# Optimization experiments

Measured on AMD Instinct MI355X. Metric: run time of the kernel, lower is better.

The kernel has to match this reference:

```python
import jax, jax.numpy as jnp
import numpy as np

WS = 7          # window size
NUM_HEADS = 8


def _depthwise_conv3x3(x, w, b):
    # x: [B, C, H, W], w: [C, 1, 3, 3], groups=C depthwise, padding=1
    y = jax.lax.conv_general_dilated(
        x, w, window_strides=(1, 1), padding='SAME',
        dimension_numbers=('NCHW', 'OIHW', 'NCHW'),
        feature_group_count=x.shape[1])
    return y + b[None, :, None, None]


def setup_inputs() -> dict:
    key = jax.random.key(0)
    k1, k2, k3 = jax.random.split(key, 3)
    B, H, W, C = 8, 112, 112, 256
    qkv = jax.random.normal(k1, (3, B, H * W, C), dtype=jnp.float32)
    lepe_w = jax.random.normal(k2, (C, 1, 3, 3), dtype=jnp.float32) * 0.1
    lepe_b = jax.random.normal(k3, (C,), dtype=jnp.float32) * 0.1
    return {"qkv": qkv, "lepe_w": lepe_w, "lepe_b": lepe_b, "H": H, "W": W}


def reference(qkv, lepe_w, lepe_b, H, W):
    q, k, v = qkv[0], qkv[1], qkv[2]          # each [B, N, C]
    B, N, C = v.shape
    hd = C // NUM_HEADS
    scale = hd ** -0.5
    Gh, Gw = H // WS, W // WS                 # H, W assumed divisible by WS

    # LePE: depthwise 3x3 conv on v viewed as image
    lepe = _depthwise_conv3x3(v.transpose(0, 2, 1).reshape(B, C, H, W), lepe_w, lepe_b)
    lepe = lepe.reshape(B, C, N).transpose(0, 2, 1)   # [B, N, C]

    def to_windows(x):
        # [B, N, C] -> [B*Gh*Gw, heads, ws*ws, hd]
        x = x.reshape(B, Gh, WS, Gw, WS, NUM_HEADS, hd)
        return x.transpose(0, 1, 3, 5, 2, 4, 6).reshape(B * Gh * Gw, NUM_HEADS, WS * WS, hd)

    qg = to_windows(q) * scale
    kg = to_windows(k)
    vg = to_windows(v)

    attn = jax.nn.softmax(jnp.einsum('ghnd,ghmd->ghnm', qg, kg), axis=-1)
    out = jnp.einsum('ghnm,ghmd->ghnd', attn, vg)     # [BG, heads, n, hd]

    # group2image: inverse window partition -> [B, N, C]
    out = out.reshape(B, Gh, Gw, NUM_HEADS, WS, WS, hd)
    out = out.transpose(0, 1, 4, 2, 5, 3, 6).reshape(B, N, C)
    return out + lepe
```

## Files before the change

### kernel.cpp

```cpp
#include <hip/hip_runtime.h>

#define WS   7
#define NH   8
#define HD   32
#define WIN  49
#define HALO 9
#define VHST 36
#define LST  34
#define UPB  4

typedef __fp16 h2  __attribute__((ext_vector_type(2)));
typedef __fp16 v4h __attribute__((ext_vector_type(4)));
typedef float  v4f __attribute__((ext_vector_type(4)));

#define WAVE_LDS_FENCE() asm volatile("s_waitcnt lgkmcnt(0)" ::: "memory")

__device__ __forceinline__ float fexp2(float x) {
    float r;
    asm("v_exp_f32 %0, %1" : "=v"(r) : "v"(x));
    return r;
}

__global__ __launch_bounds__(64 * UPB, 4)
void win_attn_lepe(const float* __restrict__ qkv,
                   const float* __restrict__ lw,
                   const float* __restrict__ lb,
                   float* __restrict__ out,
                   int B, int H, int W, int C)
{
    const int N  = H * W;
    const int Gw = W / WS;
    const int G  = (H / WS) * Gw;

    const int wave = threadIdx.x >> 6;
    const int l    = threadIdx.x & 63;

    const int unit = blockIdx.x * UPB + wave;
    const int wid  = unit >> 3;
    const int h    = unit & 7;
    const int b    = wid / G;
    const int g    = wid % G;
    const int gy   = g / Gw, gx = g % Gw;
    const int row0 = gy * WS, col0 = gx * WS;
    const int c0   = h * HD;

    const size_t plane = (size_t)B * N * C;
    const float* qb = qkv + (size_t)b * N * C;
    const float* kb = qb + plane;
    const float* vb = qb + 2 * plane;

    const int lr = l & 15;
    const int gq = l >> 4;

    __shared__ __fp16 sVh  [UPB][HALO * HALO * VHST];
    __shared__ __fp16 sW2  [UPB][16 * 20];
    __shared__ __fp16 sLepe[UPB][WIN * LST];

    for (int idx = l; idx < HALO * HALO * 8; idx += 64) {
        int p  = idx >> 3;
        int d4 = (idx & 7) * 4;
        int ry = row0 - 1 + p / HALO, rx = col0 - 1 + p % HALO;
        bool in = (ry >= 0 && ry < H && rx >= 0 && rx < W);
        float4 f = make_float4(0.f, 0.f, 0.f, 0.f);
        if (in) f = *reinterpret_cast<const float4*>(vb + ((size_t)ry * W + rx) * C + c0 + d4);
        h2 a  = __builtin_amdgcn_cvt_pkrtz(f.x, f.y);
        h2 b2 = __builtin_amdgcn_cvt_pkrtz(f.z, f.w);
        v4h v4 = { a.x, a.y, b2.x, b2.y };
        *reinterpret_cast<v4h*>(&sVh[wave][p * VHST + d4]) = v4;
    }
    for (int i = l; i < 288; i += 64) {
        int d = i / 9, t = i - d * 9;
        sW2[wave][(d >> 1) * 20 + 2 * t + (d & 1)] = (__fp16)lw[(size_t)(c0 + d) * 9 + t];
    }
    WAVE_LDS_FENCE();

    const float bias0 = lb[c0 + lr];
    const float bias1 = lb[c0 + 16 + lr];

    auto pixoff = [&](int p) -> size_t {
        p = p > 48 ? 48 : p;
        int r = row0 + p / WS, c = col0 + p % WS;
        return ((size_t)r * W + c) * C + c0;
    };

    const float scale = 0.17677669529663687f * 1.4426950408889634f;
    const float ESHIFT = 4.328085122666891f;

    v4h qf[4][2];
    #pragma unroll
    for (int m = 0; m < 4; ++m) {
        size_t off = pixoff(16 * m + lr);
        #pragma unroll
        for (int s = 0; s < 2; ++s) {
            float4 f = *reinterpret_cast<const float4*>(qb + off + 16 * s + 4 * gq);
            h2 a  = __builtin_amdgcn_cvt_pkrtz(f.x * scale, f.y * scale);
            h2 b2 = __builtin_amdgcn_cvt_pkrtz(f.z * scale, f.w * scale);
            qf[m][s] = v4h{ a.x, a.y, b2.x, b2.y };
        }
    }
    v4h kf[4][2];
    #pragma unroll
    for (int t = 0; t < 4; ++t) {
        size_t off = pixoff(16 * t + lr);
        #pragma unroll
        for (int s = 0; s < 2; ++s) {
            float4 f = *reinterpret_cast<const float4*>(kb + off + 16 * s + 4 * gq);
            h2 a  = __builtin_amdgcn_cvt_pkrtz(f.x, f.y);
            h2 b2 = __builtin_amdgcn_cvt_pkrtz(f.z, f.w);
            kf[t][s] = v4h{ a.x, a.y, b2.x, b2.y };
        }
    }

    v4h vf[4][2];
    #pragma unroll
    for (int s4 = 0; s4 < 4; ++s4) {
        #pragma unroll
        for (int j = 0; j < 4; ++j) {
            int p  = 16 * s4 + 4 * gq + j;
            int pc = p > 48 ? 48 : p;
            int hp = (pc / WS + 1) * HALO + pc % WS + 1;
            int base = hp * VHST + lr;
            vf[s4][0][j] = sVh[wave][base];
            vf[s4][1][j] = sVh[wave][base + 16];
        }
    }

    {
        h2 w2r[9];
        #pragma unroll
        for (int t = 0; t < 9; ++t)
            w2r[t] = *reinterpret_cast<const h2*>(&sW2[wave][lr * 20 + 2 * t]);
        #pragma unroll 1
        for (int it = 0; it < 13; ++it) {
            int pix = it * 4 + gq;
            if (pix < WIN) {
                int wy = pix / WS, wx = pix - (pix / WS) * WS;
                h2 acc = h2{ (__fp16)0.f, (__fp16)0.f };
                #pragma unroll
                for (int dh = 0; dh < 3; ++dh)
                    #pragma unroll
                    for (int dw = 0; dw < 3; ++dw) {
                        h2 v = *reinterpret_cast<const h2*>(
                            &sVh[wave][((wy + dh) * HALO + (wx + dw)) * VHST + 2 * lr]);
                        acc += w2r[dh * 3 + dw] * v;
                    }
                *reinterpret_cast<h2*>(&sLepe[wave][pix * LST + 2 * lr]) = acc;
            }
        }
    }
    WAVE_LDS_FENCE();

    #pragma unroll 1
    for (int mq = 0; mq < 4; ++mq) {
        v4f sa[4] = { v4f{0,0,0,0}, v4f{0,0,0,0}, v4f{0,0,0,0}, v4f{0,0,0,0} };
        #pragma unroll
        for (int tk = 0; tk < 4; ++tk)
            #pragma unroll
            for (int s = 0; s < 2; ++s)
                sa[tk] = __builtin_amdgcn_mfma_f32_16x16x16f16(kf[tk][s], qf[mq][s], sa[tk], 0, 0, 0);

        float den = 0.f;
        #pragma unroll
        for (int tk = 0; tk < 3; ++tk)
            #pragma unroll
            for (int r = 0; r < 4; ++r) {
                float e = fexp2(sa[tk][r] - ESHIFT);
                sa[tk][r] = e;
                den += e;
            }
        {
            float e0 = (gq == 0) ? fexp2(sa[3][0] - ESHIFT) : 0.f;
            sa[3][0] = e0; sa[3][1] = 0.f; sa[3][2] = 0.f; sa[3][3] = 0.f;
            den += e0;
        }
        den += __shfl_xor(den, 16);
        den += __shfl_xor(den, 32);
        const float inv = __builtin_amdgcn_rcpf(den);

        v4f oa0 = v4f{0,0,0,0}, oa1 = v4f{0,0,0,0};
        #pragma unroll
        for (int s4 = 0; s4 < 4; ++s4) {
            h2 p01 = __builtin_amdgcn_cvt_pkrtz(sa[s4][0] * inv, sa[s4][1] * inv);
            h2 p23 = __builtin_amdgcn_cvt_pkrtz(sa[s4][2] * inv, sa[s4][3] * inv);
            v4h pa = v4h{ p01.x, p01.y, p23.x, p23.y };
            oa0 = __builtin_amdgcn_mfma_f32_16x16x16f16(pa, vf[s4][0], oa0, 0, 0, 0);
            oa1 = __builtin_amdgcn_mfma_f32_16x16x16f16(pa, vf[s4][1], oa1, 0, 0, 0);
        }

        #pragma unroll
        for (int r = 0; r < 4; ++r) {
            int p = 16 * mq + 4 * gq + r;
            if (p < WIN) {
                int rr = row0 + p / WS, cc = col0 + p % WS;
                float* dst = out + ((size_t)b * N + (size_t)rr * W + cc) * C + c0 + lr;
                dst[0]  = oa0[r] + (float)sLepe[wave][p * LST + lr]      + bias0;
                dst[16] = oa1[r] + (float)sLepe[wave][p * LST + 16 + lr] + bias1;
            }
        }
    }
}

extern "C" void kernel_launch(void* const* d_in, const int* in_sizes, int n_in,
                              void* d_out, int out_size, void* d_ws, size_t ws_size,
                              hipStream_t stream) {
    const float* qkv = (const float*)d_in[0];
    const float* lw  = (const float*)d_in[1];
    const float* lb  = (const float*)d_in[2];
    float* out = (float*)d_out;

    const int H = 112, W = 112;
    const int C = in_sizes[2];
    const int N = H * W;
    const int B = in_sizes[0] / (3 * N * C);
    const int G = (H / WS) * (W / WS);

    const int units = B * G * NH;
    win_attn_lepe<<<units / UPB, 64 * UPB, 0, stream>>>(qkv, lw, lb, out, B, H, W, C);
}
```

Measured before the change: 126.4 us.

## Alias LePE output buffer onto V halo LDS and raise occupancy target

The separate per-wave LePE shared-memory array is removed, and the conv results are stored into the same buffer that holds the V halo tile. The V fragments for the PV matmul are now read from shared memory before that buffer is overwritten. The depthwise conv is split into two fully unrolled halves held in registers, with LDS fences ordering the reads of the halo before the overwriting writes. This cuts shared memory per block so more blocks fit per CU, and the launch bound minimum is raised from 4 to 6 blocks to match. The cost is more register pressure from the unrolled accumulators under a tighter register budget, which could cause spills.

Measured after the change: 138.3 us. 1.09x slower.

```diff
diff --git a/kernel.cpp b/kernel.cpp
--- a/kernel.cpp
+++ b/kernel.cpp
@@ -21,7 +21,7 @@
     return r;
 }
 
-__global__ __launch_bounds__(64 * UPB, 4)
+__global__ __launch_bounds__(64 * UPB, 6)
 void win_attn_lepe(const float* __restrict__ qkv,
                    const float* __restrict__ lw,
                    const float* __restrict__ lb,
@@ -52,9 +52,11 @@
     const int lr = l & 15;
     const int gq = l >> 4;
 
-    __shared__ __fp16 sVh  [UPB][HALO * HALO * VHST];
-    __shared__ __fp16 sW2  [UPB][16 * 20];
-    __shared__ __fp16 sLepe[UPB][WIN * LST];
+    __shared__ __fp16 sBuf[UPB][HALO * HALO * VHST];
+    __shared__ __fp16 sW2 [UPB][16 * 20];
+
+    __fp16* sVh   = &sBuf[wave][0];
+    __fp16* sLepe = &sBuf[wave][0];
 
     for (int idx = l; idx < HALO * HALO * 8; idx += 64) {
         int p  = idx >> 3;
@@ -66,7 +68,7 @@
         h2 a  = __builtin_amdgcn_cvt_pkrtz(f.x, f.y);
         h2 b2 = __builtin_amdgcn_cvt_pkrtz(f.z, f.w);
         v4h v4 = { a.x, a.y, b2.x, b2.y };
-        *reinterpret_cast<v4h*>(&sVh[wave][p * VHST + d4]) = v4;
+        *reinterpret_cast<v4h*>(&sVh[p * VHST + d4]) = v4;
     }
     for (int i = l; i < 288; i += 64) {
         int d = i / 9, t = i - d * 9;
@@ -83,6 +85,71 @@
         return ((size_t)r * W + c) * C + c0;
     };
 
+    v4h vf[4][2];
+    #pragma unroll
+    for (int s4 = 0; s4 < 4; ++s4) {
+        #pragma unroll
+        for (int j = 0; j < 4; ++j) {
+            int p  = 16 * s4 + 4 * gq + j;
+            int pc = p > 48 ? 48 : p;
+            int hp = (pc / WS + 1) * HALO + pc % WS + 1;
+            int base = hp * VHST + lr;
+            vf[s4][0][j] = sVh[base];
+            vf[s4][1][j] = sVh[base + 16];
+        }
+    }
+
+    h2 w2r[9];
+    #pragma unroll
+    for (int t = 0; t < 9; ++t)
+        w2r[t] = *reinterpret_cast<const h2*>(&sW2[wave][lr * 20 + 2 * t]);
+
+    h2 accA[7];
+    #pragma unroll
+    for (int it = 0; it < 7; ++it) {
+        int pix = it * 4 + gq;
+        int wy = pix / WS, wx = pix - (pix / WS) * WS;
+        h2 acc = h2{ (__fp16)0.f, (__fp16)0.f };
+        #pragma unroll
+        for (int dh = 0; dh < 3; ++dh)
+            #pragma unroll
+            for (int dw = 0; dw < 3; ++dw) {
+                h2 v = *reinterpret_cast<const h2*>(
+                    &sVh[((wy + dh) * HALO + (wx + dw)) * VHST + 2 * lr]);
+                acc += w2r[dh * 3 + dw] * v;
+            }
+        accA[it] = acc;
+    }
+    WAVE_LDS_FENCE();
+    #pragma unroll
+    for (int it = 0; it < 7; ++it)
+        *reinterpret_cast<h2*>(&sLepe[(it * 4 + gq) * LST + 2 * lr]) = accA[it];
+
+    h2 accB[6];
+    #pragma unroll
+    for (int it = 7; it < 13; ++it) {
+        int pix = it * 4 + gq;
+        h2 acc = h2{ (__fp16)0.f, (__fp16)0.f };
+        if (pix < WIN) {
+            int wy = pix / WS, wx = pix - (pix / WS) * WS;
+            #pragma unroll
+            for (int dh = 0; dh < 3; ++dh)
+                #pragma unroll
+                for (int dw = 0; dw < 3; ++dw) {
+                    h2 v = *reinterpret_cast<const h2*>(
+                        &sVh[((wy + dh) * HALO + (wx + dw)) * VHST + 2 * lr]);
+                    acc += w2r[dh * 3 + dw] * v;
+                }
+        }
+        accB[it - 7] = acc;
+    }
+    WAVE_LDS_FENCE();
+    #pragma unroll
+    for (int it = 7; it < 13; ++it)
+        if (it * 4 + gq < WIN)
+            *reinterpret_cast<h2*>(&sLepe[(it * 4 + gq) * LST + 2 * lr]) = accB[it - 7];
+    WAVE_LDS_FENCE();
+
     const float scale = 0.17677669529663687f * 1.4426950408889634f;
     const float ESHIFT = 4.328085122666891f;
 
@@ -110,45 +177,6 @@
             kf[t][s] = v4h{ a.x, a.y, b2.x, b2.y };
         }
     }
-
-    v4h vf[4][2];
-    #pragma unroll
-    for (int s4 = 0; s4 < 4; ++s4) {
-        #pragma unroll
-        for (int j = 0; j < 4; ++j) {
-            int p  = 16 * s4 + 4 * gq + j;
-            int pc = p > 48 ? 48 : p;
-            int hp = (pc / WS + 1) * HALO + pc % WS + 1;
-            int base = hp * VHST + lr;
-            vf[s4][0][j] = sVh[wave][base];
-            vf[s4][1][j] = sVh[wave][base + 16];
-        }
-    }
-
-    {
-        h2 w2r[9];
-        #pragma unroll
-        for (int t = 0; t < 9; ++t)
-            w2r[t] = *reinterpret_cast<const h2*>(&sW2[wave][lr * 20 + 2 * t]);
-        #pragma unroll 1
-        for (int it = 0; it < 13; ++it) {
-            int pix = it * 4 + gq;
-            if (pix < WIN) {
-                int wy = pix / WS, wx = pix - (pix / WS) * WS;
-                h2 acc = h2{ (__fp16)0.f, (__fp16)0.f };
-                #pragma unroll
-                for (int dh = 0; dh < 3; ++dh)
-                    #pragma unroll
-                    for (int dw = 0; dw < 3; ++dw) {
-                        h2 v = *reinterpret_cast<const h2*>(
-                            &sVh[wave][((wy + dh) * HALO + (wx + dw)) * VHST + 2 * lr]);
-                        acc += w2r[dh * 3 + dw] * v;
-                    }
-                *reinterpret_cast<h2*>(&sLepe[wave][pix * LST + 2 * lr]) = acc;
-            }
-        }
-    }
-    WAVE_LDS_FENCE();
 
     #pragma unroll 1
     for (int mq = 0; mq < 4; ++mq) {
@@ -193,8 +221,8 @@
             if (p < WIN) {
                 int rr = row0 + p / WS, cc = col0 + p % WS;
                 float* dst = out + ((size_t)b * N + (size_t)rr * W + cc) * C + c0 + lr;
-                dst[0]  = oa0[r] + (float)sLepe[wave][p * LST + lr]      + bias0;
-                dst[16] = oa1[r] + (float)sLepe[wave][p * LST + 16 + lr] + bias1;
+                dst[0]  = oa0[r] + (float)sLepe[p * LST + lr]      + bias0;
+                dst[16] = oa1[r] + (float)sLepe[p * LST + 16 + lr] + bias1;
             }
         }
     }
```
